# Kernel tuning notes

Measured on AMD Instinct MI355X. Metric: run time of the kernel, lower is better.

Reference implementation:

```python
import jax, jax.numpy as jnp
import numpy as np

HIDDEN = 512
HEADS = 8
HEAD_DIM = HIDDEN // HEADS


def setup_inputs() -> dict:
    key = jax.random.key(0)
    ks = jax.random.split(key, 13)
    B, S, H = 4, 2048, HIDDEN
    s = 1.0 / np.sqrt(H).astype(np.float32)
    inp = {
        "values": jax.random.normal(ks[0], (B, S, H), jnp.float32),
        "keys": jax.random.normal(ks[1], (B, S, H), jnp.float32),
        "query": jax.random.normal(ks[2], (B, S, H), jnp.float32),
        "mask": jax.random.randint(ks[3], (B, S), 0, 2, jnp.int32),
        "Wq": jax.random.normal(ks[4], (H, H), jnp.float32) * s,
        "bq": jnp.zeros((H,), jnp.float32),
        "Wk": jax.random.normal(ks[5], (H, H), jnp.float32) * s,
        "bk": jnp.zeros((H,), jnp.float32),
        "Wv": jax.random.normal(ks[6], (H, H), jnp.float32) * s,
        "bv": jnp.zeros((H,), jnp.float32),
        "Wo": jax.random.normal(ks[7], (H, H), jnp.float32) * s,
        "bo": jnp.zeros((H,), jnp.float32),
    }
    return inp


def reference(values, keys, query, mask, Wq, bq, Wk, bk, Wv, bv, Wo, bo):
    B, Sq, H = query.shape
    Sk = keys.shape[1]
    # projections (x @ W + b)
    Q = query @ Wq + bq
    K = keys @ Wk + bk
    V = values @ Wv + bv
    # [B, S, H] -> [B, heads, S, head_dim]
    def split(x, S):
        return x.reshape(B, S, HEADS, HEAD_DIM).transpose(0, 2, 1, 3)
    Qh, Kh, Vh = split(Q, Sq), split(K, Sk), split(V, Sk)
    scale = 1.0 / np.sqrt(HEAD_DIM).astype(np.float32)
    scores = jnp.einsum('bhqd,bhkd->bhqk', Qh, Kh) * scale  # [B,H,Sq,Sk]
    m = mask[:, None, None, :]  # [B,1,1,Sk]
    scores = jnp.where(m == 0, jnp.float32(-1e9), scores)
    attn = jax.nn.softmax(scores, axis=-1)
    ctx = jnp.einsum('bhqk,bhkd->bhqd', attn, Vh)
    ctx = ctx.transpose(0, 2, 1, 3).reshape(B, Sq, H)
    return ctx @ Wo + bo
```

## Files before the change

kernel.cpp:

```cpp
#include <hip/hip_runtime.h>

#define HID 512
#define NH 8
#define HD 64
#define BATCH 4
#define SEQ 2048
#define MTOT (BATCH * SEQ)

typedef unsigned short ushort_t;
typedef __bf16 bf16x8 __attribute__((ext_vector_type(8)));
typedef unsigned short ushort8v __attribute__((ext_vector_type(8)));
typedef unsigned short ushort4v __attribute__((ext_vector_type(4)));
typedef float floatx4 __attribute__((ext_vector_type(4)));
typedef unsigned int uintx4 __attribute__((ext_vector_type(4)));

static __device__ __forceinline__ unsigned short f2bf(float f) {
  __bf16 b = (__bf16)f;
  return __builtin_bit_cast(unsigned short, b);
}
static __device__ __forceinline__ float bf2f(unsigned short s) {
  union { unsigned int u; float f; } c; c.u = ((unsigned int)s) << 16;
  return c.f;
}
static __device__ __forceinline__ bf16x8 asbf(ushort8v v) {
  return __builtin_bit_cast(bf16x8, v);
}
static __device__ __forceinline__ float max3f(float a, float b, float c) {
  return fmaxf(fmaxf(a, b), c);
}
static __device__ __forceinline__ float fexp2(float x) {
  return __builtin_amdgcn_exp2f(x);
}
static __device__ __forceinline__ void gl_lds16(const ushort_t* g, ushort_t* l) {
  __builtin_amdgcn_global_load_lds(
      (const __attribute__((address_space(1))) void*)g,
      (__attribute__((address_space(3))) void*)l, 16, 0, 0);
}

#define SC_LOG2E 0.18033688011112042f

__global__ void detect_dtype(const unsigned int* __restrict__ q, int* __restrict__ flag) {
  int lane = threadIdx.x;
  int hits = 0;
#pragma unroll
  for (int i = 0; i < 4; ++i) {
    unsigned e = (q[lane * 4 + i] >> 7) & 0xff;
    hits += (e >= 110 && e <= 136) ? 1 : 0;
  }
#pragma unroll
  for (int s = 1; s < 64; s <<= 1) hits += __shfl_xor(hits, s);
  if (lane == 0) flag[0] = (hits >= 128) ? 1 : 0;
}

__global__ __launch_bounds__(256) void prep_all(
    const void* __restrict__ W0, const void* __restrict__ W1,
    const void* __restrict__ W2, const void* __restrict__ W3,
    ushort_t* __restrict__ T0, ushort_t* __restrict__ T1,
    ushort_t* __restrict__ T2, ushort_t* __restrict__ T3,
    const void* __restrict__ B0, const void* __restrict__ B1,
    const void* __restrict__ B2, const void* __restrict__ B3,
    float* __restrict__ biasF, const int* __restrict__ mask,
    float* __restrict__ mb, const int* __restrict__ flag) {
  const int bx = blockIdx.x;
  const int isbf = flag[0];
  if (bx < 256) {
    const int sel = bx >> 6, t = bx & 63;
    const void* W; ushort_t* T;
    switch (sel) {
      case 0: W = W0; T = T0; break;
      case 1: W = W1; T = T1; break;
      case 2: W = W2; T = T2; break;
      default: W = W3; T = T3; break;
    }
    __shared__ ushort_t Ts[64 * 72];
    const int tid = threadIdx.x;
    const int kt = (t >> 3) * 64;
    const int nt = (t & 7) * 64;
    const int r = tid >> 2;
    const int c = (tid & 3) * 16;

    ushort8v v0, v1;
    if (isbf) {
      const ushort_t* p = (const ushort_t*)W + (long)(kt + r) * HID + nt + c;
      v0 = *(const ushort8v*)(p);
      v1 = *(const ushort8v*)(p + 8);
    } else {
      const float* p = (const float*)W + (long)(kt + r) * HID + nt + c;
      floatx4 f0 = *(const floatx4*)(p);
      floatx4 f1 = *(const floatx4*)(p + 4);
      floatx4 f2 = *(const floatx4*)(p + 8);
      floatx4 f3 = *(const floatx4*)(p + 12);
#pragma unroll
      for (int i = 0; i < 4; ++i) {
        v0[i] = f2bf(f0[i]); v0[4 + i] = f2bf(f1[i]);
        v1[i] = f2bf(f2[i]); v1[4 + i] = f2bf(f3[i]);
      }
    }
    *(ushort8v*)(&Ts[r * 72 + c])     = v0;
    *(ushort8v*)(&Ts[r * 72 + c + 8]) = v1;
    __syncthreads();
    ushort8v o0, o1;
#pragma unroll
    for (int j = 0; j < 8; ++j) o0[j] = Ts[(c + j) * 72 + r];
#pragma unroll
    for (int j = 0; j < 8; ++j) o1[j] = Ts[(c + 8 + j) * 72 + r];
    ushort_t* q = T + (long)(nt + r) * HID + kt + c;
    *(ushort8v*)(q)     = o0;
    *(ushort8v*)(q + 8) = o1;
  } else if (bx < 264) {
    int i = (bx - 256) * 256 + threadIdx.x;
    int t = i >> 9, j = i & 511;
    const void* B = (t == 0) ? B0 : (t == 1) ? B1 : (t == 2) ? B2 : B3;
    biasF[i] = isbf ? bf2f(((const ushort_t*)B)[j]) : ((const float*)B)[j];
  } else {
    int i = (bx - 264) * 256 + threadIdx.x;
    mb[i] = mask[i] ? 0.f : -1e9f;
  }
}

__global__ __launch_bounds__(256) void gemm_qkv3(
    const void* __restrict__ X0, const void* __restrict__ X1, const void* __restrict__ X2,
    const ushort_t* __restrict__ WtBase, const float* __restrict__ biasBase,
    ushort_t* __restrict__ YBase, const int* __restrict__ flag) {
  const int isbf = flag[0];
  int lin = blockIdx.x + 256 * blockIdx.z;
  int swz = (lin & 7) * 96 + (lin >> 3);
  const int z = swz >> 8;
  const int mblk = swz & 255;
  const void* X = (z == 0) ? X0 : (z == 1) ? X1 : X2;
  const ushort_t* Wt = WtBase + (size_t)z * HID * HID;
  const float* biasF = biasBase + (size_t)z * HID;
  ushort_t* Y = YBase + (size_t)z * MTOT * HID;

  const int tid = threadIdx.x;
  const int wid = tid >> 6, lane = tid & 63;
  const int id = lane & 15, quad = lane >> 4;
  const int m0 = mblk * 32;

  __shared__ ushort_t As[32 * 32];
  __shared__ ushort_t Bs[512 * 32];

  const int a_r = tid >> 3;
  const int a_o = (tid & 1) * 4;
  const int a_pb = ((tid & 7) >> 1) ^ (a_r & 3);
  const int b_ro = lane >> 2;
  const int b_scb = (lane & 3);

  floatx4 acc[2][8];
#pragma unroll
  for (int i = 0; i < 2; ++i)
#pragma unroll
    for (int j = 0; j < 8; ++j) acc[i][j] = (floatx4){0.f, 0.f, 0.f, 0.f};

  for (int k0 = 0; k0 < HID; k0 += 32) {
    ushort4v aW;
    if (isbf) {
      aW = *(const ushort4v*)((const ushort_t*)X + (long)(m0 + a_r) * HID + k0 + (tid & 7) * 4);
    } else {
      floatx4 f = *(const floatx4*)((const float*)X + (long)(m0 + a_r) * HID + k0 + (tid & 7) * 4);
#pragma unroll
      for (int i = 0; i < 4; ++i) aW[i] = f2bf(f[i]);
    }
    __syncthreads();
    *(ushort4v*)(&As[a_r * 32 + (a_pb << 3) + a_o]) = aW;
#pragma unroll
    for (int i = 0; i < 8; ++i) {
      int rb = wid * 128 + i * 16;
      int srow = rb + b_ro;
      gl_lds16(Wt + (long)srow * HID + k0 + ((b_scb ^ (srow & 3)) << 3), &Bs[rb * 32]);
    }
    __syncthreads();
    {
      ushort8v af[2], bfv[8];
      const int pb = (quad ^ (id & 3)) << 3;
#pragma unroll
      for (int ms = 0; ms < 2; ++ms)
        af[ms] = *(const ushort8v*)(&As[(ms * 16 + id) * 32 + pb]);
#pragma unroll
      for (int ns = 0; ns < 8; ++ns)
        bfv[ns] = *(const ushort8v*)(&Bs[(wid * 128 + ns * 16 + id) * 32 + pb]);
#pragma unroll
      for (int ms = 0; ms < 2; ++ms)
#pragma unroll
        for (int ns = 0; ns < 8; ++ns)
          acc[ms][ns] = __builtin_amdgcn_mfma_f32_16x16x32_bf16(asbf(af[ms]), asbf(bfv[ns]), acc[ms][ns], 0, 0, 0);
    }
  }
#pragma unroll
  for (int ns = 0; ns < 8; ++ns) {
    int col = wid * 128 + ns * 16 + id;
    float bv = biasF[col];
#pragma unroll
    for (int ms = 0; ms < 2; ++ms) {
      int row0 = m0 + ms * 16 + quad * 4;
#pragma unroll
      for (int r = 0; r < 4; ++r)
        Y[(long)(row0 + r) * HID + col] = f2bf(acc[ms][ns][r] + bv);
    }
  }
}

__global__ __launch_bounds__(256) void gemm_out2(
    const ushort_t* __restrict__ X, const ushort_t* __restrict__ Wt,
    const float* __restrict__ biasF, void* __restrict__ out,
    const int* __restrict__ flag) {
  const int isbf = flag[0];
  const int tid = threadIdx.x;
  const int wid = tid >> 6, lane = tid & 63;
  const int id = lane & 15, quad = lane >> 4;
  const int wm = wid >> 1, wn = wid & 1;
  const int m0 = blockIdx.x * 64, n0 = blockIdx.y * 128;

  __shared__ ushort_t As[64 * 64];
  __shared__ ushort_t Bs[128 * 64];

  const int lrow = lane >> 3;
  const int scb  = (lane & 7) ^ lrow;

  floatx4 acc[2][4];
#pragma unroll
  for (int i = 0; i < 2; ++i)
#pragma unroll
    for (int j = 0; j < 4; ++j) acc[i][j] = (floatx4){0.f, 0.f, 0.f, 0.f};

  for (int k0 = 0; k0 < HID; k0 += 64) {
    __syncthreads();
#pragma unroll
    for (int i = 0; i < 2; ++i) {
      int r = wid * 16 + i * 8 + lrow;
      gl_lds16(X + (long)(m0 + r) * HID + k0 + scb * 8, &As[(wid * 16 + i * 8) * 64]);
    }
#pragma unroll
    for (int i = 0; i < 4; ++i) {
      int r = wid * 32 + i * 8 + lrow;
      gl_lds16(Wt + (long)(n0 + r) * HID + k0 + scb * 8, &Bs[(wid * 32 + i * 8) * 64]);
    }
    __syncthreads();
#pragma unroll
    for (int kk = 0; kk < 64; kk += 32) {
      ushort8v af[2], bfv[4];
      const int cb = (kk >> 3) + quad;
#pragma unroll
      for (int ms = 0; ms < 2; ++ms) {
        int row = wm * 32 + ms * 16 + id;
        af[ms] = *(const ushort8v*)(&As[row * 64 + ((cb ^ (id & 7)) << 3)]);
      }
#pragma unroll
      for (int ns = 0; ns < 4; ++ns) {
        int row = wn * 64 + ns * 16 + id;
        bfv[ns] = *(const ushort8v*)(&Bs[row * 64 + ((cb ^ (id & 7)) << 3)]);
      }
#pragma unroll
      for (int ms = 0; ms < 2; ++ms)
#pragma unroll
        for (int ns = 0; ns < 4; ++ns)
          acc[ms][ns] = __builtin_amdgcn_mfma_f32_16x16x32_bf16(asbf(af[ms]), asbf(bfv[ns]), acc[ms][ns], 0, 0, 0);
    }
  }
#pragma unroll
  for (int ns = 0; ns < 4; ++ns) {
    int col = n0 + wn * 64 + ns * 16 + id;
    float bv = biasF[col];
#pragma unroll
    for (int ms = 0; ms < 2; ++ms) {
      int row0 = m0 + wm * 32 + ms * 16 + quad * 4;
      if (isbf) {
        ushort_t* o = (ushort_t*)out;
#pragma unroll
        for (int r = 0; r < 4; ++r) o[(long)(row0 + r) * HID + col] = f2bf(acc[ms][ns][r] + bv);
      } else {
        float* o = (float*)out;
#pragma unroll
        for (int r = 0; r < 4; ++r) o[(long)(row0 + r) * HID + col] = acc[ms][ns][r] + bv;
      }
    }
  }
}

__global__ __launch_bounds__(512) void flash_attn(
    const ushort_t* __restrict__ Q, const ushort_t* __restrict__ K,
    const ushort_t* __restrict__ V, const float* __restrict__ mb,
    ushort_t* __restrict__ ctx) {
  int lin = blockIdx.x + 16 * blockIdx.y + 128 * blockIdx.z;
  int swz = (lin & 7) * 64 + (lin >> 3);
  const int qblk = swz & 15, h = (swz >> 4) & 7, b = swz >> 7;
  const int tid = threadIdx.x;
  const int wid = tid >> 6, lane = tid & 63;
  const int id = lane & 15, quad = lane >> 4;

  __shared__ ushort_t Kt[64 * 72];
  __shared__ ushort_t Vt[64 * 72];
  __shared__ ushort_t Pl[8][16 * 72];

  const ushort_t* Qb = Q + (long)(b * SEQ + qblk * 128 + wid * 16) * HID + h * HD;
  const ushort_t* Kb = K + (long)(b * SEQ) * HID + h * HD;
  const ushort_t* Vb = V + (long)(b * SEQ) * HID + h * HD;
  const float* mrow = mb + b * SEQ;

  ushort8v qf[2];
#pragma unroll
  for (int kh = 0; kh < 2; ++kh)
    qf[kh] = *(const ushort8v*)(Qb + id * HID + kh * 32 + quad * 8);

  floatx4 o[4];
  float m_i = -1e30f, l_i = 0.f;
#pragma unroll
  for (int dg = 0; dg < 4; ++dg) o[dg] = (floatx4){0, 0, 0, 0};

  const bool kstager = (tid < 256);
  const int t2 = tid & 255;
  const int skey = t2 >> 2;
  const int sdc  = (t2 & 3) * 16;
  const int vkp  = (t2 & 31) * 2;
  const int vdc  = (t2 >> 5) * 8;

  ushort8v r0, r1;
  if (kstager) {
    const ushort_t* kpp = Kb + (long)skey * HID + sdc;
    r0 = *(const ushort8v*)(kpp);
    r1 = *(const ushort8v*)(kpp + 8);
  } else {
    const ushort_t* vp0 = Vb + (long)vkp * HID + vdc;
    r0 = *(const ushort8v*)(vp0);
    r1 = *(const ushort8v*)(vp0 + HID);
  }

  for (int kb = 0; kb < SEQ / 64; ++kb) {
    if (kstager) {
      *(ushort8v*)(&Kt[skey * 72 + sdc])     = r0;
      *(ushort8v*)(&Kt[skey * 72 + sdc + 8]) = r1;
    } else {
      uintx4 a = __builtin_bit_cast(uintx4, r0);
      uintx4 bq = __builtin_bit_cast(uintx4, r1);
#pragma unroll
      for (int j = 0; j < 4; ++j) {
        unsigned int d0 = __builtin_amdgcn_perm(bq[j], a[j], 0x05040100u);
        unsigned int d1 = __builtin_amdgcn_perm(bq[j], a[j], 0x07060302u);
        *(unsigned int*)(&Vt[(vdc + 2 * j) * 72 + vkp])     = d0;
        *(unsigned int*)(&Vt[(vdc + 2 * j + 1) * 72 + vkp]) = d1;
      }
    }
    __syncthreads();

    if (kb + 1 < SEQ / 64) {
      if (kstager) {
        const ushort_t* kpp = Kb + (long)((kb + 1) * 64 + skey) * HID + sdc;
        r0 = *(const ushort8v*)(kpp);
        r1 = *(const ushort8v*)(kpp + 8);
      } else {
        const ushort_t* vp0 = Vb + (long)((kb + 1) * 64 + vkp) * HID + vdc;
        r0 = *(const ushort8v*)(vp0);
        r1 = *(const ushort8v*)(vp0 + HID);
      }
    }

    floatx4 st[4];
    __builtin_amdgcn_s_setprio(1);
#pragma unroll
    for (int ks = 0; ks < 4; ++ks) {
      ushort8v kf0 = *(const ushort8v*)(&Kt[(ks * 16 + id) * 72 + quad * 8]);
      ushort8v kf1 = *(const ushort8v*)(&Kt[(ks * 16 + id) * 72 + 32 + quad * 8]);
      floatx4 a = (floatx4){0, 0, 0, 0};
      a = __builtin_amdgcn_mfma_f32_16x16x32_bf16(asbf(kf0), asbf(qf[0]), a, 0, 0, 0);
      a = __builtin_amdgcn_mfma_f32_16x16x32_bf16(asbf(kf1), asbf(qf[1]), a, 0, 0, 0);
      st[ks] = a;
    }
    __builtin_amdgcn_s_setprio(0);
#pragma unroll
    for (int ks = 0; ks < 4; ++ks) {
      floatx4 mbv = *(const floatx4*)(mrow + kb * 64 + ks * 16 + quad * 4);
#pragma unroll
      for (int r = 0; r < 4; ++r)
        st[ks][r] = fmaf(st[ks][r], SC_LOG2E, mbv[r]);
    }
    {
      float t0 = max3f(st[0][0], st[0][1], st[0][2]);
      float t1 = max3f(st[0][3], st[1][0], st[1][1]);
      float t2m = max3f(st[1][2], st[1][3], st[2][0]);
      float t3 = max3f(st[2][1], st[2][2], st[2][3]);
      float t4 = max3f(st[3][0], st[3][1], st[3][2]);
      float mx = max3f(t0, t1, st[3][3]);
      float mz = max3f(t2m, t3, t4);
      mx = fmaxf(mx, mz);
      mx = fmaxf(mx, __shfl_xor(mx, 16));
      mx = fmaxf(mx, __shfl_xor(mx, 32));
      if (!__all(mx - m_i <= 8.f)) {
        float mnew = fmaxf(m_i, mx);
        float alpha = fexp2(m_i - mnew);
        m_i = mnew;
        l_i *= alpha;
#pragma unroll
        for (int dg = 0; dg < 4; ++dg) o[dg] *= alpha;
      }
      float mcur = m_i;
      floatx4 rsv = (floatx4){0.f, 0.f, 0.f, 0.f};
#pragma unroll
      for (int ks = 0; ks < 4; ++ks) {
        ushort4v pk;
#pragma unroll
        for (int r = 0; r < 4; ++r) {
          float p = fexp2(st[ks][r] - mcur);
          rsv[r] += p;
          pk[r] = f2bf(p);
        }
        *(ushort4v*)(&Pl[wid][id * 72 + ks * 16 + quad * 4]) = pk;
      }
      float rs = (rsv[0] + rsv[1]) + (rsv[2] + rsv[3]);
      rs += __shfl_xor(rs, 16);
      rs += __shfl_xor(rs, 32);
      l_i += rs;
    }

    __builtin_amdgcn_s_setprio(1);
#pragma unroll
    for (int kc = 0; kc < 2; ++kc) {
      ushort8v pf = *(const ushort8v*)(&Pl[wid][id * 72 + kc * 32 + quad * 8]);
#pragma unroll
      for (int dg = 0; dg < 4; ++dg) {
        ushort8v vf = *(const ushort8v*)(&Vt[(dg * 16 + id) * 72 + kc * 32 + quad * 8]);
        o[dg] = __builtin_amdgcn_mfma_f32_16x16x32_bf16(asbf(vf), asbf(pf), o[dg], 0, 0, 0);
      }
    }
    __builtin_amdgcn_s_setprio(0);
    __syncthreads();
  }

  {
    float inv = 1.0f / l_i;
    long qrow = (long)(b * SEQ + qblk * 128 + wid * 16 + id);
#pragma unroll
    for (int dg = 0; dg < 4; ++dg) {
      ushort4v pk;
#pragma unroll
      for (int r = 0; r < 4; ++r) pk[r] = f2bf(o[dg][r] * inv);
      *(ushort4v*)(&ctx[qrow * HID + h * HD + dg * 16 + quad * 4]) = pk;
    }
  }
}

extern "C" void kernel_launch(void* const* d_in, const int* in_sizes, int n_in,
                              void* d_out, int out_size, void* d_ws, size_t ws_size,
                              hipStream_t stream) {
  const void* values = d_in[0];
  const void* keys   = d_in[1];
  const void* query  = d_in[2];
  const int*  mask   = (const int*)d_in[3];
  const void* Wq = d_in[4];  const void* bq = d_in[5];
  const void* Wk = d_in[6];  const void* bk = d_in[7];
  const void* Wv = d_in[8];  const void* bv = d_in[9];
  const void* Wo = d_in[10]; const void* bo = d_in[11];

  ushort_t* ws = (ushort_t*)d_ws;
  const size_t NEL = (size_t)MTOT * HID;
  ushort_t* Qp  = ws;
  ushort_t* Kp  = ws + NEL;
  ushort_t* Vp  = ws + 2 * NEL;
  ushort_t* Cp  = ws + 3 * NEL;
  ushort_t* WqT = ws + 4 * NEL;
  ushort_t* WkT = WqT + (size_t)HID * HID;
  ushort_t* WvT = WkT + (size_t)HID * HID;
  ushort_t* WoT = WvT + (size_t)HID * HID;
  float* biasF  = (float*)(WoT + (size_t)HID * HID);
  float* mbias  = biasF + 4 * HID;
  int* flag     = (int*)(mbias + (size_t)BATCH * SEQ);

  detect_dtype<<<1, 64, 0, stream>>>((const unsigned int*)query, flag);
  prep_all<<<296, 256, 0, stream>>>(Wq, Wk, Wv, Wo, WqT, WkT, WvT, WoT,
                                    bq, bk, bv, bo, biasF, mask, mbias, flag);

  gemm_qkv3<<<dim3(MTOT / 32, 1, 3), 256, 0, stream>>>(
      query, keys, values, WqT, biasF, Qp, flag);

  flash_attn<<<dim3(SEQ / 128, NH, BATCH), 512, 0, stream>>>(Qp, Kp, Vp, mbias, Cp);

  gemm_out2<<<dim3(MTOT / 64, HID / 128), 256, 0, stream>>>(
      Cp, WoT, biasF + 3 * HID, d_out, flag);
}
```

Measured before the change: 223.9 us.

## Retile projection GEMMs to 32x128 blocks with double-buffered LDS prefetch

Both projection GEMMs now use 32x128 output tiles with a K-step of 64. The next K tile (A via registers, B via direct global-to-LDS loads) is prefetched into a second LDS buffer while MFMAs run on the current one, and a swizzled 1D grid is used. The QKV GEMM previously computed the full 512-wide N per block with a K-step of 32 and two barriers per step. This creates more, smaller blocks for better occupancy and latency hiding, and halves the barriers per K step. The cost is that the A tile is re-read from global memory four times, once per N tile, and each block does less MFMA work per load.

```diff
diff --git a/kernel.cpp b/kernel.cpp
--- a/kernel.cpp
+++ b/kernel.cpp
@@ -118,15 +118,17 @@
   }
 }
 
-__global__ __launch_bounds__(256) void gemm_qkv3(
+__global__ __launch_bounds__(256) void gemm_qkv4(
     const void* __restrict__ X0, const void* __restrict__ X1, const void* __restrict__ X2,
     const ushort_t* __restrict__ WtBase, const float* __restrict__ biasBase,
     ushort_t* __restrict__ YBase, const int* __restrict__ flag) {
   const int isbf = flag[0];
-  int lin = blockIdx.x + 256 * blockIdx.z;
-  int swz = (lin & 7) * 96 + (lin >> 3);
-  const int z = swz >> 8;
-  const int mblk = swz & 255;
+  int lin = blockIdx.x;
+  int swz = (lin & 7) * 384 + (lin >> 3);
+  const int z = swz >> 10;
+  const int rem = swz & 1023;
+  const int m0 = (rem >> 2) * 32;
+  const int n0 = (rem & 3) * 128;
   const void* X = (z == 0) ? X0 : (z == 1) ? X1 : X2;
   const ushort_t* Wt = WtBase + (size_t)z * HID * HID;
   const float* biasF = biasBase + (size_t)z * HID;
@@ -135,60 +137,89 @@
   const int tid = threadIdx.x;
   const int wid = tid >> 6, lane = tid & 63;
   const int id = lane & 15, quad = lane >> 4;
-  const int m0 = mblk * 32;
-
-  __shared__ ushort_t As[32 * 32];
-  __shared__ ushort_t Bs[512 * 32];
+
+  __shared__ ushort_t As[2][32 * 64];
+  __shared__ ushort_t Bs[2][128 * 64];
 
   const int a_r = tid >> 3;
-  const int a_o = (tid & 1) * 4;
-  const int a_pb = ((tid & 7) >> 1) ^ (a_r & 3);
-  const int b_ro = lane >> 2;
-  const int b_scb = (lane & 3);
-
-  floatx4 acc[2][8];
+  const int a_cb = tid & 7;
+  const int a_pb = a_cb ^ (a_r & 7);
+  const int b_ro = lane >> 3;
+  const int b_cb = lane & 7;
+
+  floatx4 acc[2][2];
 #pragma unroll
   for (int i = 0; i < 2; ++i)
 #pragma unroll
-    for (int j = 0; j < 8; ++j) acc[i][j] = (floatx4){0.f, 0.f, 0.f, 0.f};
-
-  for (int k0 = 0; k0 < HID; k0 += 32) {
-    ushort4v aW;
+    for (int j = 0; j < 2; ++j) acc[i][j] = (floatx4){0.f, 0.f, 0.f, 0.f};
+
+  {
+    ushort8v aW;
     if (isbf) {
-      aW = *(const ushort4v*)((const ushort_t*)X + (long)(m0 + a_r) * HID + k0 + (tid & 7) * 4);
+      aW = *(const ushort8v*)((const ushort_t*)X + (long)(m0 + a_r) * HID + a_cb * 8);
     } else {
-      floatx4 f = *(const floatx4*)((const float*)X + (long)(m0 + a_r) * HID + k0 + (tid & 7) * 4);
-#pragma unroll
-      for (int i = 0; i < 4; ++i) aW[i] = f2bf(f[i]);
-    }
+      const float* p = (const float*)X + (long)(m0 + a_r) * HID + a_cb * 8;
+      floatx4 f0 = *(const floatx4*)(p);
+      floatx4 f1 = *(const floatx4*)(p + 4);
+#pragma unroll
+      for (int i = 0; i < 4; ++i) { aW[i] = f2bf(f0[i]); aW[4 + i] = f2bf(f1[i]); }
+    }
+#pragma unroll
+    for (int i = 0; i < 4; ++i) {
+      int rb = wid * 32 + i * 8;
+      int srow = rb + b_ro;
+      gl_lds16(Wt + (long)(n0 + srow) * HID + ((b_cb ^ (srow & 7)) << 3), &Bs[0][rb * 64]);
+    }
+    *(ushort8v*)(&As[0][a_r * 64 + (a_pb << 3)]) = aW;
+  }
+  __syncthreads();
+
+  int cur = 0;
+  for (int t = 0; t < 8; ++t) {
+    const bool more = (t + 1 < 8);
+    ushort8v aW;
+    if (more) {
+      const int k1 = (t + 1) * 64;
+      if (isbf) {
+        aW = *(const ushort8v*)((const ushort_t*)X + (long)(m0 + a_r) * HID + k1 + a_cb * 8);
+      } else {
+        const float* p = (const float*)X + (long)(m0 + a_r) * HID + k1 + a_cb * 8;
+        floatx4 f0 = *(const floatx4*)(p);
+        floatx4 f1 = *(const floatx4*)(p + 4);
+#pragma unroll
+        for (int i = 0; i < 4; ++i) { aW[i] = f2bf(f0[i]); aW[4 + i] = f2bf(f1[i]); }
+      }
+#pragma unroll
+      for (int i = 0; i < 4; ++i) {
+        int rb = wid * 32 + i * 8;
+        int srow = rb + b_ro;
+        gl_lds16(Wt + (long)(n0 + srow) * HID + k1 + ((b_cb ^ (srow & 7)) << 3),
+                 &Bs[cur ^ 1][rb * 64]);
+      }
+    }
+#pragma unroll
+    for (int kk = 0; kk < 64; kk += 32) {
+      ushort8v af[2], bfv[2];
+      const int cb = (kk >> 3) + quad;
+#pragma unroll
+      for (int ms = 0; ms < 2; ++ms)
+        af[ms] = *(const ushort8v*)(&As[cur][(ms * 16 + id) * 64 + ((cb ^ (id & 7)) << 3)]);
+#pragma unroll
+      for (int ns = 0; ns < 2; ++ns)
+        bfv[ns] = *(const ushort8v*)(&Bs[cur][(wid * 32 + ns * 16 + id) * 64 + ((cb ^ (id & 7)) << 3)]);
+#pragma unroll
+      for (int ms = 0; ms < 2; ++ms)
+#pragma unroll
+        for (int ns = 0; ns < 2; ++ns)
+          acc[ms][ns] = __builtin_amdgcn_mfma_f32_16x16x32_bf16(asbf(af[ms]), asbf(bfv[ns]), acc[ms][ns], 0, 0, 0);
+    }
+    if (more) *(ushort8v*)(&As[cur ^ 1][a_r * 64 + (a_pb << 3)]) = aW;
     __syncthreads();
-    *(ushort4v*)(&As[a_r * 32 + (a_pb << 3) + a_o]) = aW;
-#pragma unroll
-    for (int i = 0; i < 8; ++i) {
-      int rb = wid * 128 + i * 16;
-      int srow = rb + b_ro;
-      gl_lds16(Wt + (long)srow * HID + k0 + ((b_scb ^ (srow & 3)) << 3), &Bs[rb * 32]);
-    }
-    __syncthreads();
-    {
-      ushort8v af[2], bfv[8];
-      const int pb = (quad ^ (id & 3)) << 3;
-#pragma unroll
-      for (int ms = 0; ms < 2; ++ms)
-        af[ms] = *(const ushort8v*)(&As[(ms * 16 + id) * 32 + pb]);
-#pragma unroll
-      for (int ns = 0; ns < 8; ++ns)
-        bfv[ns] = *(const ushort8v*)(&Bs[(wid * 128 + ns * 16 + id) * 32 + pb]);
-#pragma unroll
-      for (int ms = 0; ms < 2; ++ms)
-#pragma unroll
-        for (int ns = 0; ns < 8; ++ns)
-          acc[ms][ns] = __builtin_amdgcn_mfma_f32_16x16x32_bf16(asbf(af[ms]), asbf(bfv[ns]), acc[ms][ns], 0, 0, 0);
-    }
-  }
-#pragma unroll
-  for (int ns = 0; ns < 8; ++ns) {
-    int col = wid * 128 + ns * 16 + id;
+    cur ^= 1;
+  }
+#pragma unroll
+  for (int ns = 0; ns < 2; ++ns) {
+    int col = n0 + wid * 32 + ns * 16 + id;
     float bv = biasF[col];
 #pragma unroll
     for (int ms = 0; ms < 2; ++ms) {
@@ -200,70 +231,89 @@
   }
 }
 
-__global__ __launch_bounds__(256) void gemm_out2(
+__global__ __launch_bounds__(256) void gemm_out3(
     const ushort_t* __restrict__ X, const ushort_t* __restrict__ Wt,
     const float* __restrict__ biasF, void* __restrict__ out,
     const int* __restrict__ flag) {
   const int isbf = flag[0];
+  int lin = blockIdx.x;
+  int swz = (lin & 7) * 128 + (lin >> 3);
+  const int m0 = (swz >> 2) * 32;
+  const int n0 = (swz & 3) * 128;
+
   const int tid = threadIdx.x;
   const int wid = tid >> 6, lane = tid & 63;
   const int id = lane & 15, quad = lane >> 4;
-  const int wm = wid >> 1, wn = wid & 1;
-  const int m0 = blockIdx.x * 64, n0 = blockIdx.y * 128;
-
-  __shared__ ushort_t As[64 * 64];
-  __shared__ ushort_t Bs[128 * 64];
-
-  const int lrow = lane >> 3;
-  const int scb  = (lane & 7) ^ lrow;
-
-  floatx4 acc[2][4];
+
+  __shared__ ushort_t As[2][32 * 64];
+  __shared__ ushort_t Bs[2][128 * 64];
+
+  const int a_r = tid >> 3;
+  const int a_cb = tid & 7;
+  const int a_pb = a_cb ^ (a_r & 7);
+  const int b_ro = lane >> 3;
+  const int b_cb = lane & 7;
+
+  floatx4 acc[2][2];
 #pragma unroll
   for (int i = 0; i < 2; ++i)
 #pragma unroll
-    for (int j = 0; j < 4; ++j) acc[i][j] = (floatx4){0.f, 0.f, 0.f, 0.f};
-
-  for (int k0 = 0; k0 < HID; k0 += 64) {
+    for (int j = 0; j < 2; ++j) acc[i][j] = (floatx4){0.f, 0.f, 0.f, 0.f};
+
+  {
+    ushort8v aW = *(const ushort8v*)(X + (long)(m0 + a_r) * HID + a_cb * 8);
+#pragma unroll
+    for (int i = 0; i < 4; ++i) {
+      int rb = wid * 32 + i * 8;
+      int srow = rb + b_ro;
+      gl_lds16(Wt + (long)(n0 + srow) * HID + ((b_cb ^ (srow & 7)) << 3), &Bs[0][rb * 64]);
+    }
+    *(ushort8v*)(&As[0][a_r * 64 + (a_pb << 3)]) = aW;
+  }
+  __syncthreads();
+
+  int cur = 0;
+  for (int t = 0; t < 8; ++t) {
+    const bool more = (t + 1 < 8);
+    ushort8v aW;
+    if (more) {
+      const int k1 = (t + 1) * 64;
+      aW = *(const ushort8v*)(X + (long)(m0 + a_r) * HID + k1 + a_cb * 8);
+#pragma unroll
+      for (int i = 0; i < 4; ++i) {
+        int rb = wid * 32 + i * 8;
+        int srow = rb + b_ro;
+        gl_lds16(Wt + (long)(n0 + srow) * HID + k1 + ((b_cb ^ (srow & 7)) << 3),
+                 &Bs[cur ^ 1][rb * 64]);
+      }
+    }
+#pragma unroll
+    for (int kk = 0; kk < 64; kk += 32) {
+      ushort8v af[2], bfv[2];
+      const int cb = (kk >> 3) + quad;
+#pragma unroll
+      for (int ms = 0; ms < 2; ++ms)
+        af[ms] = *(const ushort8v*)(&As[cur][(ms * 16 + id) * 64 + ((cb ^ (id & 7)) << 3)]);
+#pragma unroll
+      for (int ns = 0; ns < 2; ++ns)
+        bfv[ns] = *(const ushort8v*)(&Bs[cur][(wid * 32 + ns * 16 + id) * 64 + ((cb ^ (id & 7)) << 3)]);
+#pragma unroll
+      for (int ms = 0; ms < 2; ++ms)
+#pragma unroll
+        for (int ns = 0; ns < 2; ++ns)
+          acc[ms][ns] = __builtin_amdgcn_mfma_f32_16x16x32_bf16(asbf(af[ms]), asbf(bfv[ns]), acc[ms][ns], 0, 0, 0);
+    }
+    if (more) *(ushort8v*)(&As[cur ^ 1][a_r * 64 + (a_pb << 3)]) = aW;
     __syncthreads();
-#pragma unroll
-    for (int i = 0; i < 2; ++i) {
-      int r = wid * 16 + i * 8 + lrow;
-      gl_lds16(X + (long)(m0 + r) * HID + k0 + scb * 8, &As[(wid * 16 + i * 8) * 64]);
-    }
-#pragma unroll
-    for (int i = 0; i < 4; ++i) {
-      int r = wid * 32 + i * 8 + lrow;
-      gl_lds16(Wt + (long)(n0 + r) * HID + k0 + scb * 8, &Bs[(wid * 32 + i * 8) * 64]);
-    }
-    __syncthreads();
-#pragma unroll
-    for (int kk = 0; kk < 64; kk += 32) {
-      ushort8v af[2], bfv[4];
-      const int cb = (kk >> 3) + quad;
-#pragma unroll
-      for (int ms = 0; ms < 2; ++ms) {
-        int row = wm * 32 + ms * 16 + id;
-        af[ms] = *(const ushort8v*)(&As[row * 64 + ((cb ^ (id & 7)) << 3)]);
-      }
-#pragma unroll
-      for (int ns = 0; ns < 4; ++ns) {
-        int row = wn * 64 + ns * 16 + id;
-        bfv[ns] = *(const ushort8v*)(&Bs[row * 64 + ((cb ^ (id & 7)) << 3)]);
-      }
-#pragma unroll
-      for (int ms = 0; ms < 2; ++ms)
-#pragma unroll
-        for (int ns = 0; ns < 4; ++ns)
-          acc[ms][ns] = __builtin_amdgcn_mfma_f32_16x16x32_bf16(asbf(af[ms]), asbf(bfv[ns]), acc[ms][ns], 0, 0, 0);
-    }
-  }
-#pragma unroll
-  for (int ns = 0; ns < 4; ++ns) {
-    int col = n0 + wn * 64 + ns * 16 + id;
+    cur ^= 1;
+  }
+#pragma unroll
+  for (int ns = 0; ns < 2; ++ns) {
+    int col = n0 + wid * 32 + ns * 16 + id;
     float bv = biasF[col];
 #pragma unroll
     for (int ms = 0; ms < 2; ++ms) {
-      int row0 = m0 + wm * 32 + ms * 16 + quad * 4;
+      int row0 = m0 + ms * 16 + quad * 4;
       if (isbf) {
         ushort_t* o = (ushort_t*)out;
 #pragma unroll
@@ -468,11 +518,9 @@
   prep_all<<<296, 256, 0, stream>>>(Wq, Wk, Wv, Wo, WqT, WkT, WvT, WoT,
                                     bq, bk, bv, bo, biasF, mask, mbias, flag);
 
-  gemm_qkv3<<<dim3(MTOT / 32, 1, 3), 256, 0, stream>>>(
-      query, keys, values, WqT, biasF, Qp, flag);
+  gemm_qkv4<<<3072, 256, 0, stream>>>(query, keys, values, WqT, biasF, Qp, flag);
 
   flash_attn<<<dim3(SEQ / 128, NH, BATCH), 512, 0, stream>>>(Qp, Kp, Vp, mbias, Cp);
 
-  gemm_out2<<<dim3(MTOT / 64, HID / 128), 256, 0, stream>>>(
-      Cp, WoT, biasF + 3 * HID, d_out, flag);
-}
+  gemm_out3<<<1024, 256, 0, stream>>>(Cp, WoT, biasF + 3 * HID, d_out, flag);
+}
```

Measured after the change: 227.6 us. No clear change (+1.6%).
